# Optimization experiments

Hardware: AMD Instinct MI355X
Metric: run time of the kernel (lower is better)

The kernel has to match this reference:

```python
import jax, jax.numpy as jnp
import numpy as np

B, L, D, H, T = 4, 1024, 1024, 16, 64


def cubic_interp_1d(vec, coords):
    # Catmull-Rom interpolation of 1D vec at real-valued coords (any shape).
    Lv = vec.shape[0]
    i = jnp.floor(coords).astype(jnp.int32)
    t = coords - i.astype(coords.dtype)
    im1 = jnp.clip(i - 1, 0, Lv - 1)
    i0 = jnp.clip(i, 0, Lv - 1)
    i1 = jnp.clip(i + 1, 0, Lv - 1)
    i2 = jnp.clip(i + 2, 0, Lv - 1)
    p0, p1, p2, p3 = vec[im1], vec[i0], vec[i1], vec[i2]
    t2 = t * t
    t3 = t2 * t
    return 0.5 * (2 * p1 + (-p0 + p2) * t + (2 * p0 - 5 * p1 + 4 * p2 - p3) * t2
                  + (-p0 + 3 * p1 - 3 * p2 + p3) * t3)


def linear_interp_1d(vec, coords):
    Lv = vec.shape[0]
    i = jnp.floor(coords).astype(jnp.int32)
    t = coords - i.astype(coords.dtype)
    i0 = jnp.clip(i, 0, Lv - 1)
    i1 = jnp.clip(i + 1, 0, Lv - 1)
    return vec[i0] * (1 - t) + vec[i1] * t


def setup_inputs() -> dict:
    key = jax.random.key(0)
    ks = jax.random.split(key, 12)
    s = 1.0 / np.sqrt(D)
    return {
        "x": jax.random.normal(ks[0], (B, L, D), jnp.float32),
        "t_enc": jax.random.normal(ks[1], (B, L, T), jnp.float32),
        "WQ": jax.random.normal(ks[2], (D, D), jnp.float32) * s,
        "WK": jax.random.normal(ks[3], (D, D), jnp.float32) * s,
        "WV": jax.random.normal(ks[4], (D, D), jnp.float32) * s,
        "WO": jax.random.normal(ks[5], (D, D), jnp.float32) * s,
        "bO": jnp.zeros((D,), jnp.float32),
        "Wt": jax.random.normal(ks[6], (T,), jnp.float32) * (1.0 / np.sqrt(T)),
        "bt": jnp.zeros((), jnp.float32),
        "p_mat": jax.random.normal(ks[7], (D, L), jnp.float32) * 0.02,
        "r_mat": jax.random.normal(ks[8], (D, L), jnp.float32) * 0.02,
        "alpha": jnp.ones((H,), jnp.float32),
        "beta": jnp.ones((H,), jnp.float32),
        "gamma": jnp.zeros((H,), jnp.float32),
    }


def reference(x, t_enc, WQ, WK, WV, WO, bO, Wt, bt, p_mat, r_mat, alpha, beta, gamma):
    Bx, Lx, Dx = x.shape
    d = Dx // H
    # projections: torch Linear y = x @ W.T
    Q = (x @ WQ.T).reshape(Bx, Lx, H, d).transpose(0, 2, 1, 3)  # [B,H,L,d]
    K = (x @ WK.T).reshape(Bx, Lx, H, d).transpose(0, 2, 1, 3)
    V = (x @ WV.T).reshape(Bx, Lx, H, d).transpose(0, 2, 1, 3)
    P = x.reshape(Bx, Lx, H, d).transpose(0, 2, 1, 3)
    # time-warped coordinates
    tau = jax.nn.sigmoid(t_enc @ Wt + bt)          # [B,L]
    coords = tau * (Lx - 1)
    # q_sca = cubic_interp(p_mat, coords).sum(-1); interp is linear in p_mat,
    # so interpolate the d-summed vector (same math, no [B,L,d] blowup).
    q_sca = cubic_interp_1d(p_mat.sum(0), coords)  # [B,L]
    delta = jnp.abs(coords[:, :, None] - coords[:, None, :])   # [B,L,L]
    r_sca = linear_interp_1d(r_mat.sum(0), delta)              # [B,L,L]
    qsum = q_sca[:, :, None] + q_sca[:, None, :]               # [B,L,L]
    Pij = jnp.einsum('bhid,bhjd->bhij', P, P)                  # [B,H,L,L]
    a = alpha[None, :, None, None]
    b = beta[None, :, None, None]
    c = gamma[None, :, None, None]
    S = a * qsum[:, None] + b * r_sca[:, None] + c
    scores = jnp.einsum('bhid,bhjd->bhij', Q, K) / jnp.sqrt(jnp.asarray(d, x.dtype)) + S * Pij
    attn = jax.nn.softmax(scores, axis=-1)
    out = jnp.einsum('bhij,bhjd->bhid', attn, V)
    out = out.transpose(0, 2, 1, 3).reshape(Bx, Lx, Dx)
    return out @ WO.T + bO
```

## Files before the change

kernel.cpp:

```cpp
#include <hip/hip_runtime.h>
#include <cstdint>
#include <cstddef>

typedef __attribute__((ext_vector_type(8))) short s8v;
typedef __attribute__((ext_vector_type(4))) float f32x4;

__device__ __forceinline__ unsigned short f2bf(float f) {
  unsigned int u = __builtin_bit_cast(unsigned int, f);
  unsigned int r = (u + 0x7fffu + ((u >> 16) & 1u)) >> 16;
  return (unsigned short)r;
}
__device__ __forceinline__ float bf2f(unsigned short s) {
  unsigned int u = ((unsigned int)s) << 16;
  return __builtin_bit_cast(float, u);
}

__device__ __forceinline__ void gload16(const void* g, void* l) {
  __builtin_amdgcn_global_load_lds(
      (const __attribute__((address_space(1))) void*)g,
      (__attribute__((address_space(3))) void*)l, 16, 0, 0);
}


__global__ __launch_bounds__(256)
void colsum_kernel(const float* __restrict__ p_mat, const float* __restrict__ r_mat,
                   float* __restrict__ q_vec, float* __restrict__ r_vec) {
  int l = blockIdx.x * 256 + threadIdx.x;
  float sp = 0.f, sr = 0.f;
  for (int d = 0; d < 1024; ++d) {
    sp += p_mat[d * 1024 + l];
    sr += r_mat[d * 1024 + l];
  }
  q_vec[l] = sp;
  r_vec[l] = sr;
}

__global__ __launch_bounds__(256)
void coords_kernel(const float* __restrict__ t_enc, const float* __restrict__ Wt,
                   const float* __restrict__ bt, const float* __restrict__ q_vec,
                   float* __restrict__ coords, float* __restrict__ q_sca) {
  int item = blockIdx.x * 4 + (threadIdx.x >> 6);
  int lane = threadIdx.x & 63;
  float v = t_enc[(size_t)item * 64 + lane] * Wt[lane];
  v += __shfl_xor(v, 32);
  v += __shfl_xor(v, 16);
  v += __shfl_xor(v, 8);
  v += __shfl_xor(v, 4);
  v += __shfl_xor(v, 2);
  v += __shfl_xor(v, 1);
  if (lane == 0) {
    float z = v + bt[0];
    float tau = 1.0f / (1.0f + expf(-z));
    float c = tau * 1023.0f;
    coords[item] = c;
    float fi = floorf(c);
    int i = (int)fi;
    float t = c - fi;
    int im1 = i - 1; if (im1 < 0) im1 = 0; if (im1 > 1023) im1 = 1023;
    int i0 = i; if (i0 < 0) i0 = 0; if (i0 > 1023) i0 = 1023;
    int i1 = i + 1; if (i1 > 1023) i1 = 1023;
    int i2 = i + 2; if (i2 > 1023) i2 = 1023;
    float p0 = q_vec[im1], p1 = q_vec[i0], p2 = q_vec[i1], p3 = q_vec[i2];
    float t2 = t * t, t3 = t2 * t;
    q_sca[item] = 0.5f * (2.f * p1 + (-p0 + p2) * t +
                          (2.f * p0 - 5.f * p1 + 4.f * p2 - p3) * t2 +
                          (-p0 + 3.f * p1 - 3.f * p2 + p3) * t3);
  }
}

__global__ __launch_bounds__(256)
void convx_kernel(const float* __restrict__ x, unsigned short* __restrict__ xb,
                  unsigned short* __restrict__ xlo) {
  int i = blockIdx.x * 256 + threadIdx.x;
  float f = x[i];
  unsigned short h = f2bf(f);
  xb[i] = h;
  xlo[i] = f2bf(f - bf2f(h));
}

__global__ __launch_bounds__(256)
void convw_kernel(const float* __restrict__ w0, const float* __restrict__ w1,
                  const float* __restrict__ w2, const float* __restrict__ w3,
                  unsigned short* __restrict__ out) {
  int i = blockIdx.x * 256 + threadIdx.x;
  int sel = i >> 20;
  const float* w = (sel == 0) ? w0 : (sel == 1) ? w1 : (sel == 2) ? w2 : w3;
  out[i] = f2bf(w[i & 0xFFFFF]);
}


__global__ __launch_bounds__(256, 2)
void gemm_qkv_kernel(const unsigned short* __restrict__ Abuf,
                     const unsigned short* __restrict__ Wb,
                     unsigned short* __restrict__ Qb,
                     unsigned short* __restrict__ Kb,
                     unsigned short* __restrict__ Vb) {
  __shared__ unsigned short As[128 * 64];
  __shared__ unsigned short Bs[128 * 64];
  const int tid = threadIdx.x, w = tid >> 6, l = tid & 63;
  const int sel = blockIdx.x >> 3;
  const int nb = (blockIdx.x & 7) * 128;
  const int m0 = blockIdx.y * 128;
  const unsigned short* Bbuf = Wb + ((size_t)sel << 20);
  const int wr = w >> 1, wc = w & 1;
  const int ll = l & 15, akg = (l >> 4) * 8;

  const f32x4 zero4 = {0.f, 0.f, 0.f, 0.f};
  f32x4 acc[4][4];
  #pragma unroll
  for (int i = 0; i < 4; ++i) {
    #pragma unroll
    for (int j = 0; j < 4; ++j) acc[i][j] = zero4;
  }

  for (int kt = 0; kt < 1024; kt += 64) {
    __syncthreads();
    #pragma unroll
    for (int q = 0; q < 4; ++q) {
      const int seg = w * 4 + q;
      const int row = seg * 8 + (l >> 3);
      const int col = kt + (l & 7) * 8;
      gload16(Abuf + (size_t)(m0 + row) * 1024 + col, &As[seg * 512 + l * 8]);
      gload16(Bbuf + (size_t)(nb + row) * 1024 + col, &Bs[seg * 512 + l * 8]);
    }
    __syncthreads();
    #pragma unroll
    for (int ks = 0; ks < 2; ++ks) {
      s8v af[4], bf[4];
      #pragma unroll
      for (int mi = 0; mi < 4; ++mi)
        af[mi] = *(const s8v*)&As[(wr * 64 + mi * 16 + ll) * 64 + ks * 32 + akg];
      #pragma unroll
      for (int ni = 0; ni < 4; ++ni)
        bf[ni] = *(const s8v*)&Bs[(wc * 64 + ni * 16 + ll) * 64 + ks * 32 + akg];
      #pragma unroll
      for (int mi = 0; mi < 4; ++mi) {
        #pragma unroll
        for (int ni = 0; ni < 4; ++ni)
          acc[mi][ni] = __builtin_amdgcn_mfma_f32_16x16x32_bf16(af[mi], bf[ni], acc[mi][ni], 0, 0, 0);
      }
    }
  }

  unsigned short* dst = (sel == 0) ? Qb : ((sel == 1) ? Kb : Vb);
  #pragma unroll
  for (int mi = 0; mi < 4; ++mi) {
    #pragma unroll
    for (int ni = 0; ni < 4; ++ni) {
      #pragma unroll
      for (int r = 0; r < 4; ++r) {
        int m = m0 + wr * 64 + mi * 16 + (l >> 4) * 4 + r;
        int ncol = nb + wc * 64 + ni * 16 + ll;
        int bb = m >> 10, lr = m & 1023, hh = ncol >> 6, dd = ncol & 63;
        dst[(((size_t)bb * 16 + hh) * 1024 + lr) * 64 + dd] = f2bf(acc[mi][ni][r]);
      }
    }
  }
}


__global__ __launch_bounds__(256, 2)
void gemm_out_kernel(const unsigned short* __restrict__ Abuf,
                     const unsigned short* __restrict__ Bbuf,
                     const float* __restrict__ bO,
                     float* __restrict__ out) {
  __shared__ unsigned short As[128 * 64];
  __shared__ unsigned short Bs[128 * 64];
  const int tid = threadIdx.x, w = tid >> 6, l = tid & 63;
  const int nb = blockIdx.x * 128;
  const int m0 = blockIdx.y * 128;
  const int wr = w >> 1, wc = w & 1;
  const int ll = l & 15, akg = (l >> 4) * 8;

  const f32x4 zero4 = {0.f, 0.f, 0.f, 0.f};
  f32x4 acc[4][4];
  #pragma unroll
  for (int i = 0; i < 4; ++i) {
    #pragma unroll
    for (int j = 0; j < 4; ++j) acc[i][j] = zero4;
  }

  for (int kt = 0; kt < 1024; kt += 64) {
    __syncthreads();
    #pragma unroll
    for (int q = 0; q < 4; ++q) {
      const int seg = w * 4 + q;
      const int row = seg * 8 + (l >> 3);
      const int col = kt + (l & 7) * 8;
      gload16(Abuf + (size_t)(m0 + row) * 1024 + col, &As[seg * 512 + l * 8]);
      gload16(Bbuf + (size_t)(nb + row) * 1024 + col, &Bs[seg * 512 + l * 8]);
    }
    __syncthreads();
    #pragma unroll
    for (int ks = 0; ks < 2; ++ks) {
      s8v af[4], bf[4];
      #pragma unroll
      for (int mi = 0; mi < 4; ++mi)
        af[mi] = *(const s8v*)&As[(wr * 64 + mi * 16 + ll) * 64 + ks * 32 + akg];
      #pragma unroll
      for (int ni = 0; ni < 4; ++ni)
        bf[ni] = *(const s8v*)&Bs[(wc * 64 + ni * 16 + ll) * 64 + ks * 32 + akg];
      #pragma unroll
      for (int mi = 0; mi < 4; ++mi) {
        #pragma unroll
        for (int ni = 0; ni < 4; ++ni)
          acc[mi][ni] = __builtin_amdgcn_mfma_f32_16x16x32_bf16(af[mi], bf[ni], acc[mi][ni], 0, 0, 0);
      }
    }
  }

  #pragma unroll
  for (int mi = 0; mi < 4; ++mi) {
    #pragma unroll
    for (int ni = 0; ni < 4; ++ni) {
      #pragma unroll
      for (int r = 0; r < 4; ++r) {
        int m = m0 + wr * 64 + mi * 16 + (l >> 4) * 4 + r;
        int ncol = nb + wc * 64 + ni * 16 + ll;
        out[(size_t)m * 1024 + ncol] = acc[mi][ni][r] + bO[ncol];
      }
    }
  }
}


__global__ __launch_bounds__(512, 2)
void attn_kernel(const unsigned short* __restrict__ Qb,
                 const unsigned short* __restrict__ Kb,
                 const unsigned short* __restrict__ Vb,
                 const unsigned short* __restrict__ xb,
                 const unsigned short* __restrict__ xlo,
                 const float* __restrict__ coords,
                 const float* __restrict__ q_sca,
                 const float* __restrict__ r_vec,
                 const float* __restrict__ alpha,
                 const float* __restrict__ beta,
                 const float* __restrict__ gamma,
                 unsigned short* __restrict__ AO) {
  __shared__ float r_s[1026];
  __shared__ unsigned short Ks[2][64 * 64];
  __shared__ unsigned short Ph[2][64 * 64];
  __shared__ unsigned short Pl[2][64 * 64];
  __shared__ unsigned short Vt[64 * 72];
  __shared__ unsigned short pbuf[8][16 * 72];

  const int tid = threadIdx.x;
  const int w = tid >> 6;
  const int l = tid & 63;
  const int gid = blockIdx.x;
  const int bh = (gid & 7) * 8 + ((gid >> 3) >> 3);
  const int xt = (gid >> 3) & 7;
  const int b = bh >> 4;
  const int h = bh & 15;
  const int iw = xt * 128 + w * 16;

  for (int t = tid; t < 1024; t += 512) r_s[t] = r_vec[t];
  if (tid < 2) r_s[1024 + tid] = r_vec[1023];

  const float INVLN2 = 1.4426950408889634f;
  const float a_h = alpha[h] * INVLN2, b_h = beta[h] * INVLN2, c_h = gamma[h] * INVLN2;
  const int lg = l >> 4;
  const int ll = l & 15;
  const int rowg = lg * 4;
  const int akg = lg * 8;

  float aqi[4], ci[4];
  #pragma unroll
  for (int r = 0; r < 4; ++r) {
    aqi[r] = fmaf(a_h, q_sca[b * 1024 + iw + rowg + r], c_h);
    ci[r] = coords[b * 1024 + iw + rowg + r];
  }

  s8v qf[2], pih[2], pil[2];
  {
    const unsigned short* qp = Qb + ((size_t)bh * 1024 + iw + ll) * 64 + akg;
    qf[0] = *(const s8v*)(qp);
    qf[1] = *(const s8v*)(qp + 32);
    const unsigned short* xp = xb + ((size_t)b * 1024 + iw + ll) * 1024 + h * 64 + akg;
    pih[0] = *(const s8v*)(xp);
    pih[1] = *(const s8v*)(xp + 32);
    const unsigned short* xq = xlo + ((size_t)b * 1024 + iw + ll) * 1024 + h * 64 + akg;
    pil[0] = *(const s8v*)(xq);
    pil[1] = *(const s8v*)(xq + 32);
  }

  const f32x4 zero4 = {0.f, 0.f, 0.f, 0.f};
  f32x4 o[4];
  #pragma unroll
  for (int ds = 0; ds < 4; ++ds) o[ds] = zero4;
  float mrow[4], lsum[4];
  #pragma unroll
  for (int r = 0; r < 4; ++r) { mrow[r] = -3.0e38f; lsum[r] = 0.f; }

  unsigned short* pw = pbuf[w];
  const int cs = (((l & 7) ^ ((l >> 3) & 7)) * 8);
  const int srow = l >> 3;

  auto stage = [&](int j0, int buf) {
    const int row = w * 8 + srow;
    gload16(Kb + ((size_t)bh * 1024 + j0 + row) * 64 + cs, &Ks[buf][w * 512 + l * 8]);
    gload16(xb + ((size_t)b * 1024 + j0 + row) * 1024 + h * 64 + cs, &Ph[buf][w * 512 + l * 8]);
    gload16(xlo + ((size_t)b * 1024 + j0 + row) * 1024 + h * 64 + cs, &Pl[buf][w * 512 + l * 8]);
  };
  auto vload = [&](int j0) -> s8v {
    return *(const s8v*)(Vb + ((size_t)bh * 1024 + j0 + l) * 64 + w * 8);
  };
  auto vwrite = [&](const s8v& vv) {
    #pragma unroll
    for (int e = 0; e < 8; ++e) Vt[(w * 8 + e) * 72 + l] = (unsigned short)vv[e];
  };

  stage(0, 0);
  s8v vv0 = vload(0);
  stage(64, 1);
  s8v vv1 = vload(64);
  vwrite(vv0);
  __syncthreads();

#define ATTN_TILE(T, PAR, VCONS, VPROD)                                          \
  {                                                                              \
    const int j0 = (T) * 64;                                                     \
    float cj[4], aqj[4];                                                         \
    _Pragma("unroll")                                                            \
    for (int s = 0; s < 4; ++s) {                                                \
      cj[s] = coords[b * 1024 + j0 + ll + 16 * s];                               \
      aqj[s] = a_h * q_sca[b * 1024 + j0 + ll + 16 * s];                         \
    }                                                                            \
    f32x4 aqk[4], app[4];                                                        \
    _Pragma("unroll")                                                            \
    for (int s = 0; s < 4; ++s) { aqk[s] = zero4; app[s] = zero4; }              \
    _Pragma("unroll")                                                            \
    for (int ks = 0; ks < 2; ++ks) {                                             \
      _Pragma("unroll")                                                          \
      for (int s = 0; s < 4; ++s) {                                              \
        const int rb = (ll + 16 * s) * 64 + (((ks * 4 + lg) ^ (ll & 7)) * 8);    \
        s8v kf = *(const s8v*)&Ks[PAR][rb];                                      \
        s8v hf = *(const s8v*)&Ph[PAR][rb];                                      \
        s8v lf = *(const s8v*)&Pl[PAR][rb];                                      \
        aqk[s] = __builtin_amdgcn_mfma_f32_16x16x32_bf16(qf[ks], kf, aqk[s], 0, 0, 0);   \
        app[s] = __builtin_amdgcn_mfma_f32_16x16x32_bf16(pih[ks], hf, app[s], 0, 0, 0);  \
        app[s] = __builtin_amdgcn_mfma_f32_16x16x32_bf16(pih[ks], lf, app[s], 0, 0, 0);  \
        app[s] = __builtin_amdgcn_mfma_f32_16x16x32_bf16(pil[ks], hf, app[s], 0, 0, 0);  \
      }                                                                          \
    }                                                                            \
    float tmax[4];                                                               \
    _Pragma("unroll")                                                            \
    for (int r = 0; r < 4; ++r) tmax[r] = -3.0e38f;                              \
    _Pragma("unroll")                                                            \
    for (int s = 0; s < 4; ++s) {                                                \
      _Pragma("unroll")                                                          \
      for (int r = 0; r < 4; ++r) {                                              \
        float delta = fabsf(ci[r] - cj[s]);                                      \
        int i0 = (int)delta;                                                     \
        float tt = delta - (float)i0;                                            \
        float r0 = r_s[i0];                                                      \
        float r1 = r_s[i0 + 1];                                                  \
        float rs = fmaf(tt, r1 - r0, r0);                                        \
        float S = fmaf(b_h, rs, aqi[r] + aqj[s]);                                \
        float v = fmaf(0.18033688f, aqk[s][r], S * app[s][r]);                   \
        app[s][r] = v;                                                           \
        tmax[r] = fmaxf(tmax[r], v);                                             \
      }                                                                          \
    }                                                                            \
    _Pragma("unroll")                                                            \
    for (int r = 0; r < 4; ++r) {                                                \
      float v = tmax[r];                                                         \
      v = fmaxf(v, __shfl_xor(v, 1));                                            \
      v = fmaxf(v, __shfl_xor(v, 2));                                            \
      v = fmaxf(v, __shfl_xor(v, 4));                                            \
      v = fmaxf(v, __shfl_xor(v, 8));                                            \
      float mn = fmaxf(mrow[r], v);                                              \
      float scale = exp2f(mrow[r] - mn);                                         \
      mrow[r] = mn;                                                              \
      lsum[r] *= scale;                                                          \
      o[0][r] *= scale; o[1][r] *= scale; o[2][r] *= scale; o[3][r] *= scale;    \
    }                                                                            \
    _Pragma("unroll")                                                            \
    for (int s = 0; s < 4; ++s) {                                                \
      _Pragma("unroll")                                                          \
      for (int r = 0; r < 4; ++r) {                                              \
        float e = exp2f(app[s][r] - mrow[r]);                                    \
        lsum[r] += e;                                                            \
        pw[(rowg + r) * 72 + ll + 16 * s] = f2bf(e);                             \
      }                                                                          \
    }                                                                            \
    _Pragma("unroll")                                                            \
    for (int ks = 0; ks < 2; ++ks) {                                             \
      s8v pa = *(const s8v*)&pw[ll * 72 + ks * 32 + akg];                        \
      _Pragma("unroll")                                                          \
      for (int dq = 0; dq < 4; ++dq) {                                           \
        s8v vf = *(const s8v*)&Vt[(ll + 16 * dq) * 72 + ks * 32 + akg];          \
        o[dq] = __builtin_amdgcn_mfma_f32_16x16x32_bf16(pa, vf, o[dq], 0, 0, 0); \
      }                                                                          \
    }                                                                            \
    __syncthreads();                          \
    if ((T) < 15) {                                                              \
      vwrite(VCONS);                                           \
      if ((T) < 14) {                                                            \
        stage((T) + 2 > 15 ? 0 : ((T) + 2) * 64, PAR);                           \
        VPROD = vload(((T) + 2) * 64);                                           \
      }                                                                          \
      asm volatile("s_waitcnt lgkmcnt(0)" ::: "memory");                         \
      __builtin_amdgcn_sched_barrier(0);                                         \
      __builtin_amdgcn_s_barrier();                                              \
    }                                                                            \
  }

  for (int t2 = 0; t2 < 16; t2 += 2) {
    ATTN_TILE(t2, 0, vv1, vv0);
    ATTN_TILE(t2 + 1, 1, vv0, vv1);
  }
#undef ATTN_TILE

  #pragma unroll
  for (int r = 0; r < 4; ++r) {
    float v = lsum[r];
    v += __shfl_xor(v, 1);
    v += __shfl_xor(v, 2);
    v += __shfl_xor(v, 4);
    v += __shfl_xor(v, 8);
    lsum[r] = 1.0f / v;
  }
  #pragma unroll
  for (int ds = 0; ds < 4; ++ds) {
    #pragma unroll
    for (int r = 0; r < 4; ++r) {
      AO[((size_t)b * 1024 + iw + rowg + r) * 1024 + h * 64 + ll + 16 * ds] =
          f2bf(o[ds][r] * lsum[r]);
    }
  }
}


extern "C" void kernel_launch(void* const* d_in, const int* in_sizes, int n_in,
                              void* d_out, int out_size, void* d_ws, size_t ws_size,
                              hipStream_t stream) {
  const float* x     = (const float*)d_in[0];
  const float* t_enc = (const float*)d_in[1];
  const float* WQ    = (const float*)d_in[2];
  const float* WK    = (const float*)d_in[3];
  const float* WV    = (const float*)d_in[4];
  const float* WO    = (const float*)d_in[5];
  const float* bO    = (const float*)d_in[6];
  const float* Wt    = (const float*)d_in[7];
  const float* bt    = (const float*)d_in[8];
  const float* p_mat = (const float*)d_in[9];
  const float* r_mat = (const float*)d_in[10];
  const float* alpha = (const float*)d_in[11];
  const float* beta  = (const float*)d_in[12];
  const float* gamma = (const float*)d_in[13];
  float* out = (float*)d_out;

  char* ws = (char*)d_ws;
  unsigned short* xb  = (unsigned short*)(ws + ((size_t)0 << 20));
  unsigned short* xlo = (unsigned short*)(ws + ((size_t)8 << 20));
  unsigned short* wb  = (unsigned short*)(ws + ((size_t)16 << 20));
  unsigned short* Qb  = (unsigned short*)(ws + ((size_t)24 << 20));
  unsigned short* Kb  = (unsigned short*)(ws + ((size_t)32 << 20));
  unsigned short* Vb  = (unsigned short*)(ws + ((size_t)40 << 20));
  unsigned short* AO  = (unsigned short*)(ws + ((size_t)48 << 20));
  float* q_vec  = (float*)(ws + ((size_t)56 << 20));
  float* r_vec  = q_vec + 1024;
  float* coords = r_vec + 1024;
  float* q_sca  = coords + 4096;

  colsum_kernel<<<4, 256, 0, stream>>>(p_mat, r_mat, q_vec, r_vec);
  coords_kernel<<<1024, 256, 0, stream>>>(t_enc, Wt, bt, q_vec, coords, q_sca);
  convx_kernel<<<16384, 256, 0, stream>>>(x, xb, xlo);
  convw_kernel<<<16384, 256, 0, stream>>>(WQ, WK, WV, WO, wb);
  gemm_qkv_kernel<<<dim3(24, 32), 256, 0, stream>>>(xb, wb, Qb, Kb, Vb);
  attn_kernel<<<512, 512, 0, stream>>>(Qb, Kb, Vb, xb, xlo, coords, q_sca,
                                       r_vec, alpha, beta, gamma, AO);
  gemm_out_kernel<<<dim3(8, 32), 256, 0, stream>>>(AO, wb + ((size_t)3 << 20), bO, out);
}
```

Measured before the change: 332.1 us.

## Parallelize colsum, fuse conversions, double-buffer GEMMs, coalesce QKV stores, raise MFMA priority

Splits the column-sum over 32 d-chunks with atomic adds into a zeroed buffer, so the reduction is no longer a serial loop over only 4 blocks. Merges the x and weight bf16 conversion kernels into one launch. Double-buffers the LDS tiles in both GEMMs so the next tile loads while the current one is computed. Stages the QKV epilogue through LDS so stores are 16-byte vectors instead of scattered 2-byte writes. Wraps MFMA sections in s_setprio. The trade-offs are doubled LDS use, which may cut occupancy, and an extra memset launch.

```diff
diff --git a/kernel.cpp b/kernel.cpp
--- a/kernel.cpp
+++ b/kernel.cpp
@@ -25,14 +25,15 @@
 __global__ __launch_bounds__(256)
 void colsum_kernel(const float* __restrict__ p_mat, const float* __restrict__ r_mat,
                    float* __restrict__ q_vec, float* __restrict__ r_vec) {
-  int l = blockIdx.x * 256 + threadIdx.x;
+  int col = blockIdx.x * 256 + threadIdx.x;
+  int d0 = blockIdx.y * 32;
   float sp = 0.f, sr = 0.f;
-  for (int d = 0; d < 1024; ++d) {
-    sp += p_mat[d * 1024 + l];
-    sr += r_mat[d * 1024 + l];
-  }
-  q_vec[l] = sp;
-  r_vec[l] = sr;
+  for (int d = d0; d < d0 + 32; ++d) {
+    sp += p_mat[d * 1024 + col];
+    sr += r_mat[d * 1024 + col];
+  }
+  atomicAdd(&q_vec[col], sp);
+  atomicAdd(&r_vec[col], sr);
 }
 
 __global__ __launch_bounds__(256)
@@ -69,23 +70,24 @@
 }
 
 __global__ __launch_bounds__(256)
-void convx_kernel(const float* __restrict__ x, unsigned short* __restrict__ xb,
-                  unsigned short* __restrict__ xlo) {
-  int i = blockIdx.x * 256 + threadIdx.x;
-  float f = x[i];
-  unsigned short h = f2bf(f);
-  xb[i] = h;
-  xlo[i] = f2bf(f - bf2f(h));
-}
-
-__global__ __launch_bounds__(256)
-void convw_kernel(const float* __restrict__ w0, const float* __restrict__ w1,
-                  const float* __restrict__ w2, const float* __restrict__ w3,
-                  unsigned short* __restrict__ out) {
-  int i = blockIdx.x * 256 + threadIdx.x;
-  int sel = i >> 20;
-  const float* w = (sel == 0) ? w0 : (sel == 1) ? w1 : (sel == 2) ? w2 : w3;
-  out[i] = f2bf(w[i & 0xFFFFF]);
+void conv_all_kernel(const float* __restrict__ x,
+                     const float* __restrict__ w0, const float* __restrict__ w1,
+                     const float* __restrict__ w2, const float* __restrict__ w3,
+                     unsigned short* __restrict__ xb, unsigned short* __restrict__ xlo,
+                     unsigned short* __restrict__ wb) {
+  int bx = blockIdx.x;
+  if (bx < 16384) {
+    int i = bx * 256 + threadIdx.x;
+    float f = x[i];
+    unsigned short h = f2bf(f);
+    xb[i] = h;
+    xlo[i] = f2bf(f - bf2f(h));
+  } else {
+    int i = (bx - 16384) * 256 + threadIdx.x;
+    int sel = i >> 20;
+    const float* w = (sel == 0) ? w0 : (sel == 1) ? w1 : (sel == 2) ? w2 : w3;
+    wb[i] = f2bf(w[i & 0xFFFFF]);
+  }
 }
 
 
@@ -95,15 +97,15 @@
                      unsigned short* __restrict__ Qb,
                      unsigned short* __restrict__ Kb,
                      unsigned short* __restrict__ Vb) {
-  __shared__ unsigned short As[128 * 64];
-  __shared__ unsigned short Bs[128 * 64];
+  __shared__ unsigned short As[2][128 * 64];
+  __shared__ unsigned short Bs[2][128 * 64];
   const int tid = threadIdx.x, w = tid >> 6, l = tid & 63;
   const int sel = blockIdx.x >> 3;
   const int nb = (blockIdx.x & 7) * 128;
   const int m0 = blockIdx.y * 128;
   const unsigned short* Bbuf = Wb + ((size_t)sel << 20);
   const int wr = w >> 1, wc = w & 1;
-  const int ll = l & 15, akg = (l >> 4) * 8;
+  const int ll = l & 15, lg = l >> 4, akg = lg * 8;
 
   const f32x4 zero4 = {0.f, 0.f, 0.f, 0.f};
   f32x4 acc[4][4];
@@ -113,48 +115,62 @@
     for (int j = 0; j < 4; ++j) acc[i][j] = zero4;
   }
 
-  for (int kt = 0; kt < 1024; kt += 64) {
-    __syncthreads();
+  auto stage = [&](int kt, int buf) {
     #pragma unroll
     for (int q = 0; q < 4; ++q) {
       const int seg = w * 4 + q;
       const int row = seg * 8 + (l >> 3);
-      const int col = kt + (l & 7) * 8;
-      gload16(Abuf + (size_t)(m0 + row) * 1024 + col, &As[seg * 512 + l * 8]);
-      gload16(Bbuf + (size_t)(nb + row) * 1024 + col, &Bs[seg * 512 + l * 8]);
-    }
+      const int col = kt * 64 + (l & 7) * 8;
+      gload16(Abuf + (size_t)(m0 + row) * 1024 + col, &As[buf][seg * 512 + l * 8]);
+      gload16(Bbuf + (size_t)(nb + row) * 1024 + col, &Bs[buf][seg * 512 + l * 8]);
+    }
+  };
+
+  stage(0, 0);
+  for (int kt = 0; kt < 16; ++kt) {
     __syncthreads();
+    if (kt < 15) stage(kt + 1, (kt + 1) & 1);
+    const int bb = kt & 1;
     #pragma unroll
     for (int ks = 0; ks < 2; ++ks) {
       s8v af[4], bf[4];
       #pragma unroll
       for (int mi = 0; mi < 4; ++mi)
-        af[mi] = *(const s8v*)&As[(wr * 64 + mi * 16 + ll) * 64 + ks * 32 + akg];
+        af[mi] = *(const s8v*)&As[bb][(wr * 64 + mi * 16 + ll) * 64 + ks * 32 + akg];
       #pragma unroll
       for (int ni = 0; ni < 4; ++ni)
-        bf[ni] = *(const s8v*)&Bs[(wc * 64 + ni * 16 + ll) * 64 + ks * 32 + akg];
+        bf[ni] = *(const s8v*)&Bs[bb][(wc * 64 + ni * 16 + ll) * 64 + ks * 32 + akg];
+      __builtin_amdgcn_s_setprio(1);
       #pragma unroll
       for (int mi = 0; mi < 4; ++mi) {
         #pragma unroll
         for (int ni = 0; ni < 4; ++ni)
           acc[mi][ni] = __builtin_amdgcn_mfma_f32_16x16x32_bf16(af[mi], bf[ni], acc[mi][ni], 0, 0, 0);
       }
+      __builtin_amdgcn_s_setprio(0);
     }
   }
 
   unsigned short* dst = (sel == 0) ? Qb : ((sel == 1) ? Kb : Vb);
+  unsigned short* ch = &As[0][0];
+  const int err = tid >> 3;
+  const int ecb = tid & 7;
   #pragma unroll
   for (int mi = 0; mi < 4; ++mi) {
+    __syncthreads();
     #pragma unroll
     for (int ni = 0; ni < 4; ++ni) {
       #pragma unroll
-      for (int r = 0; r < 4; ++r) {
-        int m = m0 + wr * 64 + mi * 16 + (l >> 4) * 4 + r;
-        int ncol = nb + wc * 64 + ni * 16 + ll;
-        int bb = m >> 10, lr = m & 1023, hh = ncol >> 6, dd = ncol & 63;
-        dst[(((size_t)bb * 16 + hh) * 1024 + lr) * 64 + dd] = f2bf(acc[mi][ni][r]);
-      }
-    }
+      for (int r = 0; r < 4; ++r)
+        ch[(wr * 16 + lg * 4 + r) * 136 + wc * 64 + ni * 16 + ll] = f2bf(acc[mi][ni][r]);
+    }
+    __syncthreads();
+    int m = m0 + (err >> 4) * 64 + mi * 16 + (err & 15);
+    int ncol = nb + ecb * 16;
+    int bb2 = m >> 10, lr = m & 1023, hh = ncol >> 6, dd = ncol & 63;
+    unsigned short* gp = &dst[(((size_t)bb2 * 16 + hh) * 1024 + lr) * 64 + dd];
+    *(s8v*)(gp)     = *(const s8v*)&ch[err * 136 + ecb * 16];
+    *(s8v*)(gp + 8) = *(const s8v*)&ch[err * 136 + ecb * 16 + 8];
   }
 }
 
@@ -164,8 +180,8 @@
                      const unsigned short* __restrict__ Bbuf,
                      const float* __restrict__ bO,
                      float* __restrict__ out) {
-  __shared__ unsigned short As[128 * 64];
-  __shared__ unsigned short Bs[128 * 64];
+  __shared__ unsigned short As[2][128 * 64];
+  __shared__ unsigned short Bs[2][128 * 64];
   const int tid = threadIdx.x, w = tid >> 6, l = tid & 63;
   const int nb = blockIdx.x * 128;
   const int m0 = blockIdx.y * 128;
@@ -180,32 +196,39 @@
     for (int j = 0; j < 4; ++j) acc[i][j] = zero4;
   }
 
-  for (int kt = 0; kt < 1024; kt += 64) {
-    __syncthreads();
+  auto stage = [&](int kt, int buf) {
     #pragma unroll
     for (int q = 0; q < 4; ++q) {
       const int seg = w * 4 + q;
       const int row = seg * 8 + (l >> 3);
-      const int col = kt + (l & 7) * 8;
-      gload16(Abuf + (size_t)(m0 + row) * 1024 + col, &As[seg * 512 + l * 8]);
-      gload16(Bbuf + (size_t)(nb + row) * 1024 + col, &Bs[seg * 512 + l * 8]);
-    }
+      const int col = kt * 64 + (l & 7) * 8;
+      gload16(Abuf + (size_t)(m0 + row) * 1024 + col, &As[buf][seg * 512 + l * 8]);
+      gload16(Bbuf + (size_t)(nb + row) * 1024 + col, &Bs[buf][seg * 512 + l * 8]);
+    }
+  };
+
+  stage(0, 0);
+  for (int kt = 0; kt < 16; ++kt) {
     __syncthreads();
+    if (kt < 15) stage(kt + 1, (kt + 1) & 1);
+    const int bb = kt & 1;
     #pragma unroll
     for (int ks = 0; ks < 2; ++ks) {
       s8v af[4], bf[4];
       #pragma unroll
       for (int mi = 0; mi < 4; ++mi)
-        af[mi] = *(const s8v*)&As[(wr * 64 + mi * 16 + ll) * 64 + ks * 32 + akg];
+        af[mi] = *(const s8v*)&As[bb][(wr * 64 + mi * 16 + ll) * 64 + ks * 32 + akg];
       #pragma unroll
       for (int ni = 0; ni < 4; ++ni)
-        bf[ni] = *(const s8v*)&Bs[(wc * 64 + ni * 16 + ll) * 64 + ks * 32 + akg];
+        bf[ni] = *(const s8v*)&Bs[bb][(wc * 64 + ni * 16 + ll) * 64 + ks * 32 + akg];
+      __builtin_amdgcn_s_setprio(1);
       #pragma unroll
       for (int mi = 0; mi < 4; ++mi) {
         #pragma unroll
         for (int ni = 0; ni < 4; ++ni)
           acc[mi][ni] = __builtin_amdgcn_mfma_f32_16x16x32_bf16(af[mi], bf[ni], acc[mi][ni], 0, 0, 0);
       }
+      __builtin_amdgcn_s_setprio(0);
     }
   }
 
@@ -337,10 +360,12 @@
         s8v kf = *(const s8v*)&Ks[PAR][rb];                                      \
         s8v hf = *(const s8v*)&Ph[PAR][rb];                                      \
         s8v lf = *(const s8v*)&Pl[PAR][rb];                                      \
+        __builtin_amdgcn_s_setprio(1);                                           \
         aqk[s] = __builtin_amdgcn_mfma_f32_16x16x32_bf16(qf[ks], kf, aqk[s], 0, 0, 0);   \
         app[s] = __builtin_amdgcn_mfma_f32_16x16x32_bf16(pih[ks], hf, app[s], 0, 0, 0);  \
         app[s] = __builtin_amdgcn_mfma_f32_16x16x32_bf16(pih[ks], lf, app[s], 0, 0, 0);  \
         app[s] = __builtin_amdgcn_mfma_f32_16x16x32_bf16(pil[ks], hf, app[s], 0, 0, 0);  \
+        __builtin_amdgcn_s_setprio(0);                                           \
       }                                                                          \
     }                                                                            \
     float tmax[4];                                                               \
@@ -387,11 +412,13 @@
     _Pragma("unroll")                                                            \
     for (int ks = 0; ks < 2; ++ks) {                                             \
       s8v pa = *(const s8v*)&pw[ll * 72 + ks * 32 + akg];                        \
+      __builtin_amdgcn_s_setprio(1);                                             \
       _Pragma("unroll")                                                          \
       for (int dq = 0; dq < 4; ++dq) {                                           \
         s8v vf = *(const s8v*)&Vt[(ll + 16 * dq) * 72 + ks * 32 + akg];          \
         o[dq] = __builtin_amdgcn_mfma_f32_16x16x32_bf16(pa, vf, o[dq], 0, 0, 0); \
       }                                                                          \
+      __builtin_amdgcn_s_setprio(0);                                             \
     }                                                                            \
     __syncthreads();                          \
     if ((T) < 15) {                                                              \
@@ -464,10 +491,10 @@
   float* coords = r_vec + 1024;
   float* q_sca  = coords + 4096;
 
-  colsum_kernel<<<4, 256, 0, stream>>>(p_mat, r_mat, q_vec, r_vec);
+  hipMemsetAsync(q_vec, 0, 2048 * sizeof(float), stream);
+  colsum_kernel<<<dim3(4, 32), 256, 0, stream>>>(p_mat, r_mat, q_vec, r_vec);
   coords_kernel<<<1024, 256, 0, stream>>>(t_enc, Wt, bt, q_vec, coords, q_sca);
-  convx_kernel<<<16384, 256, 0, stream>>>(x, xb, xlo);
-  convw_kernel<<<16384, 256, 0, stream>>>(WQ, WK, WV, WO, wb);
+  conv_all_kernel<<<32768, 256, 0, stream>>>(x, WQ, WK, WV, WO, xb, xlo, wb);
   gemm_qkv_kernel<<<dim3(24, 32), 256, 0, stream>>>(xb, wb, Qb, Kb, Vb);
   attn_kernel<<<512, 512, 0, stream>>>(Qb, Kb, Vb, xb, xlo, coords, q_sca,
                                        r_vec, alpha, beta, gamma, AO);
```

Result: faster. 289.8 us (-12.7%).
